# Kernel tuning notes

Measured on AMD Instinct MI355X. Metric: run time of the kernel, lower is better.

## Reference

```python
import jax, jax.numpy as jnp
import numpy as np

BS, NA, NC, G = 64, 3, 80, 44
IMG = 352
STRIDE = IMG / G  # 8.0
ANCHORS = np.array([[10.0, 13.0], [16.0, 30.0], [33.0, 23.0]], dtype=np.float32)
SCALED_ANCHORS = ANCHORS / STRIDE  # anchors in grid units


def setup_inputs() -> dict:
    key = jax.random.key(0)
    x = jax.random.normal(key, (BS, NA * (5 + NC), G, G), dtype=jnp.float32)
    return {"x": x}


def reference(x):
    bs = x.shape[0]
    # [bs, nA, 5+nC, H, W] -> [bs, nA, H, W, 5+nC]
    pred = x.reshape(bs, NA, 5 + NC, G, G).transpose(0, 1, 3, 4, 2)
    px = jax.nn.sigmoid(pred[..., 0])
    py = jax.nn.sigmoid(pred[..., 1])
    pw = pred[..., 2]
    ph = pred[..., 3]
    conf = jax.nn.sigmoid(pred[..., 4])
    pred_cls = jax.nn.sigmoid(pred[..., 5:])

    grid = jnp.arange(G, dtype=jnp.float32)
    grid_x = grid[None, None, None, :]          # broadcast over W
    grid_y = grid[None, None, :, None]          # broadcast over H
    aw = jnp.asarray(SCALED_ANCHORS[:, 0])[None, :, None, None]
    ah = jnp.asarray(SCALED_ANCHORS[:, 1])[None, :, None, None]

    bx = px + grid_x
    by = py + grid_y
    bw = jnp.exp(pw) * aw
    bh = jnp.exp(ph) * ah
    pred_boxes = jnp.stack([bx, by, bw, bh], axis=-1)  # [bs,nA,H,W,4]

    out = jnp.concatenate(
        [
            pred_boxes.reshape(bs, -1, 4) * jnp.float32(STRIDE),
            conf.reshape(bs, -1, 1),
            pred_cls.reshape(bs, -1, NC),
        ],
        axis=-1,
    )  # [bs, nA*G*G, 5+nC]
    return out
```

## Files before the change

kernel.cpp:

```cpp
#include <hip/hip_runtime.h>


#define BSZ      64
#define NA       3
#define NC       80
#define GRID     44
#define SPATIAL  (GRID * GRID)
#define CH       (5 + NC)
#define TILE     64
#define TILES_PER_BA ((SPATIAL + TILE - 1) / TILE)
#define NF       (CH * (TILE / 4))
#define NITER    ((NF + 255) / 256)
#define STRIDE_F 8.0f
#define NXCD     8
#define NWG      (BSZ * NA * TILES_PER_BA)
#define CHUNK    (NWG / NXCD)

typedef float vfloat4 __attribute__((ext_vector_type(4)));

__device__ __forceinline__ float sigf(float x) {
    return 1.0f / (1.0f + __expf(-x));
}

__global__ __launch_bounds__(256, 4)
void yolo_kernel(const float* __restrict__ in, float* __restrict__ out) {
    __shared__ float tile[TILE * CH];

    const int bid0 = blockIdx.x;
    const int bid  = (bid0 % NXCD) * CHUNK + bid0 / NXCD;

    const int t   = bid % TILES_PER_BA;
    const int ba  = bid / TILES_PER_BA;
    const int a   = ba % NA;

    const int s0    = t * TILE;
    const int valid = min(TILE, SPATIAL - s0);

    const float aw = (a == 0) ? 10.0f : (a == 1) ? 16.0f : 33.0f;
    const float ah = (a == 0) ? 13.0f : (a == 1) ? 30.0f : 23.0f;

    const int tid = threadIdx.x;
    const float* inbase = in + (size_t)ba * CH * SPATIAL + s0;

    float4 v[NITER];
    #pragma unroll
    for (int i = 0; i < NITER; ++i) {
        int f = tid + i * 256;
        int c = f >> 4, q = f & 15;
        if (f < NF && q * 4 < valid)
            v[i] = *(const float4*)(inbase + (size_t)c * SPATIAL + q * 4);
    }

    #pragma unroll
    for (int i = 0; i < NITER; ++i) {
        int f = tid + i * 256;
        int c = f >> 4, q = f & 15;
        if (f >= NF || q * 4 >= valid) continue;
        float r[4] = {v[i].x, v[i].y, v[i].z, v[i].w};
        #pragma unroll
        for (int j = 0; j < 4; ++j) {
            int   sl = q * 4 + j;
            int   gs = s0 + sl;
            float x  = r[j];
            float o;
            if (c == 0)      o = (sigf(x) + (float)(gs % GRID)) * STRIDE_F;
            else if (c == 1) o = (sigf(x) + (float)(gs / GRID)) * STRIDE_F;
            else if (c == 2) o = __expf(x) * aw;
            else if (c == 3) o = __expf(x) * ah;
            else             o = sigf(x);
            tile[sl * CH + c] = o;
        }
    }
    __syncthreads();

    const size_t obase = ((size_t)ba * SPATIAL + s0) * CH;
    const int total = valid * CH;
    for (int k4 = tid * 4; k4 < total; k4 += 1024) {
        vfloat4 w = *(const vfloat4*)(tile + k4);
        *(vfloat4*)(out + obase + k4) = w;
    }
}

extern "C" void kernel_launch(void* const* d_in, const int* in_sizes, int n_in,
                              void* d_out, int out_size, void* d_ws, size_t ws_size,
                              hipStream_t stream) {
    const float* in = (const float*)d_in[0];
    float* out = (float*)d_out;
    yolo_kernel<<<NWG, 256, 0, stream>>>(in, out);
}
```

Measured before the change: 228.3 us.

## Process six tiles per block with two-deep register prefetch of input loads

Each workgroup now handles six consecutive tiles instead of one, and keeps loads for the next two tiles in flight in registers while it transforms and flushes the current tile through shared memory. Load indices are clamped so loads are unconditional. The aim is to hide global load latency and cut per-block launch overhead. In exchange it needs more registers, which may lower occupancy, adds extra barriers per tile, and leaves fewer blocks to spread across CUs.

```diff
diff --git a/kernel.cpp b/kernel.cpp
--- a/kernel.cpp
+++ b/kernel.cpp
@@ -8,13 +8,14 @@
 #define SPATIAL  (GRID * GRID)
 #define CH       (5 + NC)
 #define TILE     64
-#define TILES_PER_BA ((SPATIAL + TILE - 1) / TILE)
+#define TPB      31
+#define NTL      (BSZ * NA * TPB)
+#define NT       6
+#define NBLK     (NTL / NT)
+#define NXCD     8
+#define CHUNKB   (NBLK / NXCD)
 #define NF       (CH * (TILE / 4))
-#define NITER    ((NF + 255) / 256)
 #define STRIDE_F 8.0f
-#define NXCD     8
-#define NWG      (BSZ * NA * TILES_PER_BA)
-#define CHUNK    (NWG / NXCD)
 
 typedef float vfloat4 __attribute__((ext_vector_type(4)));
 
@@ -22,62 +23,98 @@
     return 1.0f / (1.0f + __expf(-x));
 }
 
+struct TileCtx { int s0, valid, ba; float aw, ah; };
+
+__device__ __forceinline__ TileCtx tctx(int T) {
+    TileCtx tc;
+    int t    = T % TPB;
+    tc.ba    = T / TPB;
+    tc.s0    = t * TILE;
+    tc.valid = min(TILE, SPATIAL - tc.s0);
+    int a = tc.ba % NA;
+    tc.aw = (a == 0) ? 10.0f : (a == 1) ? 16.0f : 33.0f;
+    tc.ah = (a == 0) ? 13.0f : (a == 1) ? 30.0f : 23.0f;
+    return tc;
+}
+
+__device__ __forceinline__ void issue(const float* __restrict__ in,
+                                      const TileCtx& tc, int tid,
+                                      float4 (&v)[6]) {
+    const float* ib = in + (size_t)tc.ba * CH * SPATIAL + tc.s0;
+    #pragma unroll
+    for (int i = 0; i < 6; ++i) {
+        int f = tid + i * 256;
+        int c = min(f >> 4, CH - 1);
+        int off = min((f & 15) * 4, tc.valid - 4);
+        v[i] = *(const float4*)(ib + (size_t)c * SPATIAL + off);
+    }
+}
+
+__device__ __forceinline__ void transform(const TileCtx& tc, int tid,
+                                          const float4 (&v)[6],
+                                          float* __restrict__ tile) {
+    #pragma unroll
+    for (int i = 0; i < 6; ++i) {
+        int f = tid + i * 256;
+        int c = f >> 4, q = f & 15;
+        if (f >= NF || q * 4 >= tc.valid) continue;
+        float r[4] = {v[i].x, v[i].y, v[i].z, v[i].w};
+        #pragma unroll
+        for (int j = 0; j < 4; ++j) {
+            int   sl = q * 4 + j;
+            int   gs = tc.s0 + sl;
+            float x  = r[j];
+            float o;
+            if (c == 0)      o = (sigf(x) + (float)(gs % GRID)) * STRIDE_F;
+            else if (c == 1) o = (sigf(x) + (float)(gs / GRID)) * STRIDE_F;
+            else if (c == 2) o = __expf(x) * tc.aw;
+            else if (c == 3) o = __expf(x) * tc.ah;
+            else             o = sigf(x);
+            tile[sl * CH + c] = o;
+        }
+    }
+}
+
+__device__ __forceinline__ void flush(float* __restrict__ out,
+                                      const TileCtx& tc, int tid,
+                                      const float* __restrict__ tile) {
+    const size_t ob = ((size_t)tc.ba * SPATIAL + tc.s0) * (size_t)CH;
+    const int total = tc.valid * CH;
+    for (int k4 = tid * 4; k4 < total; k4 += 1024) {
+        vfloat4 w = *(const vfloat4*)(tile + k4);
+        *(vfloat4*)(out + ob + k4) = w;
+    }
+}
+
 __global__ __launch_bounds__(256, 4)
 void yolo_kernel(const float* __restrict__ in, float* __restrict__ out) {
     __shared__ float tile[TILE * CH];
 
     const int bid0 = blockIdx.x;
-    const int bid  = (bid0 % NXCD) * CHUNK + bid0 / NXCD;
+    const int bid  = (bid0 % NXCD) * CHUNKB + bid0 / NXCD;
+    const int tid  = threadIdx.x;
+    const int T0   = bid * NT;
 
-    const int t   = bid % TILES_PER_BA;
-    const int ba  = bid / TILES_PER_BA;
-    const int a   = ba % NA;
-
-    const int s0    = t * TILE;
-    const int valid = min(TILE, SPATIAL - s0);
-
-    const float aw = (a == 0) ? 10.0f : (a == 1) ? 16.0f : 33.0f;
-    const float ah = (a == 0) ? 13.0f : (a == 1) ? 30.0f : 23.0f;
-
-    const int tid = threadIdx.x;
-    const float* inbase = in + (size_t)ba * CH * SPATIAL + s0;
-
-    float4 v[NITER];
-    #pragma unroll
-    for (int i = 0; i < NITER; ++i) {
-        int f = tid + i * 256;
-        int c = f >> 4, q = f & 15;
-        if (f < NF && q * 4 < valid)
-            v[i] = *(const float4*)(inbase + (size_t)c * SPATIAL + q * 4);
-    }
+    float4 v0[6], v1[6], v2[6];
+    TileCtx t0 = tctx(T0);
+    TileCtx t1 = tctx(T0 + 1);
+    TileCtx t2;
+    issue(in, t0, tid, v0);
+    issue(in, t1, tid, v1);
 
     #pragma unroll
-    for (int i = 0; i < NITER; ++i) {
-        int f = tid + i * 256;
-        int c = f >> 4, q = f & 15;
-        if (f >= NF || q * 4 >= valid) continue;
-        float r[4] = {v[i].x, v[i].y, v[i].z, v[i].w};
+    for (int k = 0; k < NT; ++k) {
+        if (k + 2 < NT) {
+            t2 = tctx(T0 + k + 2);
+            issue(in, t2, tid, v2);
+        }
+        transform(t0, tid, v0, tile);
+        __syncthreads();
+        flush(out, t0, tid, tile);
+        if (k + 1 < NT) __syncthreads();
+        t0 = t1; t1 = t2;
         #pragma unroll
-        for (int j = 0; j < 4; ++j) {
-            int   sl = q * 4 + j;
-            int   gs = s0 + sl;
-            float x  = r[j];
-            float o;
-            if (c == 0)      o = (sigf(x) + (float)(gs % GRID)) * STRIDE_F;
-            else if (c == 1) o = (sigf(x) + (float)(gs / GRID)) * STRIDE_F;
-            else if (c == 2) o = __expf(x) * aw;
-            else if (c == 3) o = __expf(x) * ah;
-            else             o = sigf(x);
-            tile[sl * CH + c] = o;
-        }
-    }
-    __syncthreads();
-
-    const size_t obase = ((size_t)ba * SPATIAL + s0) * CH;
-    const int total = valid * CH;
-    for (int k4 = tid * 4; k4 < total; k4 += 1024) {
-        vfloat4 w = *(const vfloat4*)(tile + k4);
-        *(vfloat4*)(out + obase + k4) = w;
+        for (int i = 0; i < 6; ++i) { v0[i] = v1[i]; v1[i] = v2[i]; }
     }
 }
 
@@ -86,5 +123,5 @@
                               hipStream_t stream) {
     const float* in = (const float*)d_in[0];
     float* out = (float*)d_out;
-    yolo_kernel<<<NWG, 256, 0, stream>>>(in, out);
+    yolo_kernel<<<NBLK, 256, 0, stream>>>(in, out);
 }
```

Measured after the change: 232.7 us. About the same (+2.0%).
